# Performance work log

Measured on AMD Instinct MI355X. Metric: run time of the kernel, lower is better.

Reference implementation:

```python
import jax, jax.numpy as jnp
import numpy as np

DIM = 512
HEADS = 8
DIM_HEAD = 64
B, N = 4, 2048
EPS = 1e-5


def setup_inputs() -> dict:
    key = jax.random.key(0)
    ks = jax.random.split(key, 6)
    s = 0.02
    x = jax.random.normal(ks[0], (B, N, DIM), dtype=jnp.float32)
    Wq = jax.random.normal(ks[1], (DIM, HEADS * DIM_HEAD), dtype=jnp.float32) * s
    Wkv = jax.random.normal(ks[2], (DIM, 2 * HEADS * DIM_HEAD), dtype=jnp.float32) * s
    Wo = jax.random.normal(ks[3], (HEADS * DIM_HEAD, DIM), dtype=jnp.float32) * s
    bo = jnp.zeros((DIM,), dtype=jnp.float32)
    # gating layer: torch init is weight=0, bias=1; randomize weight slightly for a nontrivial path
    Wg = jax.random.normal(ks[4], (DIM, HEADS * DIM_HEAD), dtype=jnp.float32) * s
    bg = jnp.ones((HEADS * DIM_HEAD,), dtype=jnp.float32)
    gamma = jnp.ones((DIM,), dtype=jnp.float32)
    beta = jnp.zeros((DIM,), dtype=jnp.float32)
    return {"x": x, "Wq": Wq, "Wkv": Wkv, "Wo": Wo, "bo": bo,
            "Wg": Wg, "bg": bg, "gamma": gamma, "beta": beta}


def reference(x, Wq, Wkv, Wo, bo, Wg, bg, gamma, beta):
    h, d = HEADS, DIM_HEAD
    scale = d ** -0.5
    b, n, _ = x.shape

    q = x @ Wq                                   # [b, n, h*d]
    kv = x @ Wkv                                 # [b, n, 2*h*d]
    k, v = jnp.split(kv, 2, axis=-1)

    def split_heads(t):
        return t.reshape(b, n, h, d).transpose(0, 2, 1, 3)  # [b, h, n, d]

    q = split_heads(q) * scale
    k = split_heads(k)
    v = split_heads(v)

    dots = jnp.einsum('bhid,bhjd->bhij', q, k)   # [b, h, n, n]
    attn = jax.nn.softmax(dots, axis=-1)
    out = jnp.einsum('bhij,bhjd->bhid', attn, v)  # [b, h, n, d]
    out = out.transpose(0, 2, 1, 3).reshape(b, n, h * d)

    gates = x @ Wg + bg                           # [b, n, h*d]
    out = out * jax.nn.sigmoid(gates)
    out = out @ Wo + bo                           # [b, n, dim]
    out = x + out

    # LayerNorm over last dim, eps=1e-5 (torch default)
    mu = jnp.mean(out, axis=-1, keepdims=True)
    var = jnp.var(out, axis=-1, keepdims=True)
    out = (out - mu) * jax.lax.rsqrt(var + EPS) * gamma + beta
    return out
```

## Files before the change

### kernel.cpp

```cpp
#include <hip/hip_runtime.h>
#include <hip/hip_bf16.h>
#include <stdint.h>
#include <stddef.h>

#define SEQ   2048
#define NBATCH 4
#define NHEAD  8
#define DMODEL 512

typedef __attribute__((ext_vector_type(8))) short bf16x8;
typedef __attribute__((ext_vector_type(4))) float f32x4;
typedef __attribute__((ext_vector_type(16))) float f32x16;

#define MFMA16(a, b, c) __builtin_amdgcn_mfma_f32_16x16x32_bf16(a, b, c, 0, 0, 0)
#define MFMA32(a, b, c) __builtin_amdgcn_mfma_f32_32x32x16_bf16(a, b, c, 0, 0, 0)

#define QSCALE 0.18033688011112042f

__device__ __forceinline__ float bf2f(ushort u) {
  union { uint32_t i; float f; } v; v.i = ((uint32_t)u) << 16; return v.f;
}
__device__ __forceinline__ ushort f2bf(float f) {
  union { float f; uint32_t i; } v; v.f = f;
  uint32_t u = v.i;
  return (ushort)((u + 0x7fffu + ((u >> 16) & 1u)) >> 16);
}
__device__ __forceinline__ uint32_t cvtpk(float lo, float hi) {
  uint32_t d;
  asm("v_cvt_pk_bf16_f32 %0, %1, %2" : "=v"(d) : "v"(lo), "v"(hi));
  return d;
}

#if __has_builtin(__builtin_amdgcn_global_load_lds)
__device__ __forceinline__ void gload16(const void* g, void* l) {
  __builtin_amdgcn_global_load_lds(
      (const __attribute__((address_space(1))) void*)g,
      (__attribute__((address_space(3))) void*)l, 16, 0, 0);
}
#define GLOAD_DIRECT 1
#else
#define GLOAD_DIRECT 0
#endif

__global__ __launch_bounds__(256) void cvt_k(const float* __restrict__ in,
                                             ushort* __restrict__ out, int n8) {
  int i = blockIdx.x * 256 + threadIdx.x;
  if (i >= n8) return;
  const float4* p = (const float4*)(in + (size_t)i * 8);
  float4 a = p[0], b = p[1];
  union { int4 v; ushort u[8]; } o;
  o.u[0] = f2bf(a.x); o.u[1] = f2bf(a.y); o.u[2] = f2bf(a.z); o.u[3] = f2bf(a.w);
  o.u[4] = f2bf(b.x); o.u[5] = f2bf(b.y); o.u[6] = f2bf(b.z); o.u[7] = f2bf(b.w);
  *(int4*)(out + (size_t)i * 8) = o.v;
}

__global__ __launch_bounds__(256) void wtrans_k(const float* __restrict__ Wq,
                                                const float* __restrict__ Wkv,
                                                const float* __restrict__ Wg,
                                                const float* __restrict__ Wo,
                                                ushort* __restrict__ WT,
                                                ushort* __restrict__ WoT) {
  __shared__ ushort tile[32][33];
  int bx = blockIdx.x;
  const float* W;
  ushort* dst;
  int N, nt;
  if (bx < 16)       { W = Wq;  dst = WT;              N = 512;  nt = bx; }
  else if (bx < 48)  { W = Wkv; dst = WT + 512 * 512;  N = 1024; nt = bx - 16; }
  else if (bx < 64)  { W = Wg;  dst = WT + 1536 * 512; N = 512;  nt = bx - 48; }
  else               { W = Wo;  dst = WoT;             N = 512;  nt = bx - 64; }
  int t = threadIdx.x;
  int n0 = nt * 32, k0 = blockIdx.y * 32;
  int r = t >> 3, c = (t & 7) * 4;
#pragma unroll
  for (int j = 0; j < 4; j++)
    tile[r][c + j] = f2bf(W[(size_t)(k0 + r) * N + n0 + c + j]);
  __syncthreads();
#pragma unroll
  for (int j = 0; j < 4; j++)
    dst[(size_t)(n0 + r) * 512 + k0 + c + j] = tile[c + j][r];
}

__global__ __launch_bounds__(256, 2) void gemm128_k(const ushort* __restrict__ A,
                                                    const ushort* __restrict__ Bt,
                                                    ushort* __restrict__ qb,
                                                    ushort* __restrict__ kb,
                                                    ushort* __restrict__ vT,
                                                    ushort* __restrict__ gsb,
                                                    const float* __restrict__ bias) {
  __shared__ __align__(16) ushort Sh[4 * 128 * 64];
#define ASB(p) (Sh + (p) * (128 * 64))
#define BSB(p) (Sh + 2 * (128 * 64) + (p) * (128 * 64))
  int t = threadIdx.x;
  int nb = gridDim.x * gridDim.y;
  int bid = blockIdx.y * gridDim.x + blockIdx.x;
  int swz = (bid & 7) * (nb >> 3) + (bid >> 3);
  int row0 = (swz / gridDim.x) * 128, col0 = (swz % gridDim.x) * 128;

  int w = t >> 6, l = t & 63, l31 = l & 31, hi = l >> 5;
  int wm = w >> 1, wn = w & 1;
  f32x16 acc[2][2] = {};

  int srow = t >> 3;
  int ssl = (t & 7) ^ (srow & 7);
  const ushort* Ag = A + (size_t)(row0 + srow) * 512 + ssl * 8;
  const ushort* Bg = Bt + (size_t)(col0 + srow) * 512 + ssl * 8;
  int wslot = __builtin_amdgcn_readfirstlane((t >> 6) << 6);

#if GLOAD_DIRECT
#define STG(p, kt)                                                              \
  do {                                                                          \
    gload16(Ag + (size_t)(kt) * 64 + 0 * 32 * 512, ASB(p) + (wslot +   0) * 8); \
    gload16(Ag + (size_t)(kt) * 64 + 1 * 32 * 512, ASB(p) + (wslot + 256) * 8); \
    gload16(Ag + (size_t)(kt) * 64 + 2 * 32 * 512, ASB(p) + (wslot + 512) * 8); \
    gload16(Ag + (size_t)(kt) * 64 + 3 * 32 * 512, ASB(p) + (wslot + 768) * 8); \
    gload16(Bg + (size_t)(kt) * 64 + 0 * 32 * 512, BSB(p) + (wslot +   0) * 8); \
    gload16(Bg + (size_t)(kt) * 64 + 1 * 32 * 512, BSB(p) + (wslot + 256) * 8); \
    gload16(Bg + (size_t)(kt) * 64 + 2 * 32 * 512, BSB(p) + (wslot + 512) * 8); \
    gload16(Bg + (size_t)(kt) * 64 + 3 * 32 * 512, BSB(p) + (wslot + 768) * 8); \
  } while (0)
#else
#define STG(p, kt)                                                                  \
  do {                                                                              \
    *(int4*)(ASB(p) + (t +   0) * 8) = *(const int4*)(Ag + (size_t)(kt) * 64);      \
    *(int4*)(ASB(p) + (t + 256) * 8) =                                              \
        *(const int4*)(Ag + (size_t)(kt) * 64 + 1 * 32 * 512);                      \
    *(int4*)(ASB(p) + (t + 512) * 8) =                                              \
        *(const int4*)(Ag + (size_t)(kt) * 64 + 2 * 32 * 512);                      \
    *(int4*)(ASB(p) + (t + 768) * 8) =                                              \
        *(const int4*)(Ag + (size_t)(kt) * 64 + 3 * 32 * 512);                      \
    *(int4*)(BSB(p) + (t +   0) * 8) = *(const int4*)(Bg + (size_t)(kt) * 64);      \
    *(int4*)(BSB(p) + (t + 256) * 8) =                                              \
        *(const int4*)(Bg + (size_t)(kt) * 64 + 1 * 32 * 512);                      \
    *(int4*)(BSB(p) + (t + 512) * 8) =                                              \
        *(const int4*)(Bg + (size_t)(kt) * 64 + 2 * 32 * 512);                      \
    *(int4*)(BSB(p) + (t + 768) * 8) =                                              \
        *(const int4*)(Bg + (size_t)(kt) * 64 + 3 * 32 * 512);                      \
  } while (0)
#endif

#define FRAG(Mb, r, s) \
  (*(const bf16x8*)(Mb + ((r) * 64) + ((((s) ^ ((r) & 7))) << 3)))

  STG(0, 0);
  __syncthreads();

  for (int kt = 0; kt < 8; kt++) {
    int p = kt & 1;
    if (kt < 7) STG(p ^ 1, kt + 1);

    bf16x8 bfrag[2][4];
#pragma unroll
    for (int cb = 0; cb < 2; cb++)
#pragma unroll
      for (int kk = 0; kk < 4; kk++)
        bfrag[cb][kk] = FRAG(BSB(p), wn * 64 + cb * 32 + l31, kk * 2 + hi);

    __builtin_amdgcn_s_setprio(1);
#pragma unroll
    for (int rb = 0; rb < 2; rb++) {
      bf16x8 af[4];
#pragma unroll
      for (int kk = 0; kk < 4; kk++)
        af[kk] = FRAG(ASB(p), wm * 64 + rb * 32 + l31, kk * 2 + hi);
#pragma unroll
      for (int kk = 0; kk < 4; kk++) {
        acc[rb][0] = MFMA32(af[kk], bfrag[0][kk], acc[rb][0]);
        acc[rb][1] = MFMA32(af[kk], bfrag[1][kk], acc[rb][1]);
      }
    }
    __builtin_amdgcn_s_setprio(0);

    if (kt < 7) __syncthreads();
  }
#undef STG
#undef FRAG

  if (col0 >= 1024 && col0 < 1536) {
    __syncthreads();
    ushort* lt = Sh;
#pragma unroll
    for (int rb = 0; rb < 2; rb++)
#pragma unroll
      for (int cb = 0; cb < 2; cb++)
#pragma unroll
        for (int e = 0; e < 16; e++) {
          int rr = (e & 3) + 8 * (e >> 2) + 4 * hi;
          int rowL = wm * 64 + rb * 32 + rr;
          int colL = wn * 64 + cb * 32 + l31;
          lt[colL * 136 + rowL] = f2bf(acc[rb][cb][e]);
        }
    __syncthreads();
    int b_ = row0 >> 11;
    int nb0 = row0 & 2047;
#pragma unroll
    for (int r = 0; r < 8; r++) {
      int lin = r * 256 + t;
      int dcol = lin >> 4, n8 = lin & 15;
      int vcol = (col0 - 1024) + dcol;
      int hh = vcol >> 6, dd = vcol & 63;
      bf16x8 v = *(const bf16x8*)(lt + dcol * 136 + n8 * 8);
      *(bf16x8*)(vT + (((size_t)(b_ * 8 + hh) * 64) + dd) * 2048 + nb0 + n8 * 8) = v;
    }
  } else {
#pragma unroll
    for (int rb = 0; rb < 2; rb++) {
#pragma unroll
      for (int cb = 0; cb < 2; cb++) {
#pragma unroll
        for (int e = 0; e < 16; e++) {
          int rr = (e & 3) + 8 * (e >> 2) + 4 * hi;
          int row = row0 + wm * 64 + rb * 32 + rr;
          int col = col0 + wn * 64 + cb * 32 + l31;
          float v = acc[rb][cb][e];
          if (col0 < 512) {
            qb[(size_t)row * 512 + col] = f2bf(v * QSCALE);
          } else if (col0 < 1024) {
            kb[(size_t)row * 512 + (col - 512)] = f2bf(v);
          } else {
            v += bias[col - 1536];
            v = 1.f / (1.f + __expf(-v));
            gsb[(size_t)row * 512 + (col - 1536)] = f2bf(v);
          }
        }
      }
    }
  }
#undef ASB
#undef BSB
}

__global__ __launch_bounds__(256, 2) void gemm_o_k(const ushort* __restrict__ A,
                                                   const ushort* __restrict__ Bt,
                                                   float* __restrict__ yout,
                                                   const float* __restrict__ bias,
                                                   const float* __restrict__ res) {
  __shared__ __align__(16) ushort As[2][128 * 64];
  __shared__ __align__(16) ushort Bs[2][64 * 64];
  int t = threadIdx.x;
  int nb = gridDim.x * gridDim.y;
  int bid = blockIdx.y * gridDim.x + blockIdx.x;
  int swz = (bid & 7) * (nb >> 3) + (bid >> 3);
  int row0 = (swz / gridDim.x) * 128, col0 = (swz % gridDim.x) * 64;

  int w = t >> 6, l = t & 63, l31 = l & 31, hi = l >> 5;
  int wm = w >> 1, wn = w & 1;
  f32x16 acc[2] = {};

  int srow = t >> 3;
  int ssl = (t & 7) ^ (srow & 7);
  const ushort* Ag = A + (size_t)(row0 + srow) * 512 + ssl * 8;
  const ushort* Bg = Bt + (size_t)(col0 + srow) * 512 + ssl * 8;
  int wslot = __builtin_amdgcn_readfirstlane((t >> 6) << 6);

#if GLOAD_DIRECT
#define STG(p, kt)                                                                \
  do {                                                                            \
    gload16(Ag + (size_t)(kt) * 64 + 0 * 32 * 512, &As[p][(wslot +   0) * 8]);    \
    gload16(Ag + (size_t)(kt) * 64 + 1 * 32 * 512, &As[p][(wslot + 256) * 8]);    \
    gload16(Ag + (size_t)(kt) * 64 + 2 * 32 * 512, &As[p][(wslot + 512) * 8]);    \
    gload16(Ag + (size_t)(kt) * 64 + 3 * 32 * 512, &As[p][(wslot + 768) * 8]);    \
    gload16(Bg + (size_t)(kt) * 64 + 0 * 32 * 512, &Bs[p][(wslot +   0) * 8]);    \
    gload16(Bg + (size_t)(kt) * 64 + 1 * 32 * 512, &Bs[p][(wslot + 256) * 8]);    \
  } while (0)
#else
#define STG(p, kt)                                                                  \
  do {                                                                              \
    *(int4*)(&As[p][(t +   0) * 8]) = *(const int4*)(Ag + (size_t)(kt) * 64);       \
    *(int4*)(&As[p][(t + 256) * 8]) =                                               \
        *(const int4*)(Ag + (size_t)(kt) * 64 + 1 * 32 * 512);                      \
    *(int4*)(&As[p][(t + 512) * 8]) =                                               \
        *(const int4*)(Ag + (size_t)(kt) * 64 + 2 * 32 * 512);                      \
    *(int4*)(&As[p][(t + 768) * 8]) =                                               \
        *(const int4*)(Ag + (size_t)(kt) * 64 + 3 * 32 * 512);                      \
    *(int4*)(&Bs[p][(t +   0) * 8]) = *(const int4*)(Bg + (size_t)(kt) * 64);       \
    *(int4*)(&Bs[p][(t + 256) * 8]) =                                               \
        *(const int4*)(Bg + (size_t)(kt) * 64 + 1 * 32 * 512);                      \
  } while (0)
#endif

#define FRAG(Mb, r, s) \
  (*(const bf16x8*)(&(Mb)[((r) * 64) + ((((s) ^ ((r) & 7))) << 3)]))

  STG(0, 0);
  __syncthreads();

  for (int kt = 0; kt < 8; kt++) {
    int p = kt & 1;
    if (kt < 7) STG(p ^ 1, kt + 1);

    bf16x8 bfrag[4];
#pragma unroll
    for (int kk = 0; kk < 4; kk++)
      bfrag[kk] = FRAG(Bs[p], wn * 32 + l31, kk * 2 + hi);

    __builtin_amdgcn_s_setprio(1);
#pragma unroll
    for (int rb = 0; rb < 2; rb++) {
      bf16x8 af[4];
#pragma unroll
      for (int kk = 0; kk < 4; kk++)
        af[kk] = FRAG(As[p], wm * 64 + rb * 32 + l31, kk * 2 + hi);
#pragma unroll
      for (int kk = 0; kk < 4; kk++)
        acc[rb] = MFMA32(af[kk], bfrag[kk], acc[rb]);
    }
    __builtin_amdgcn_s_setprio(0);

    if (kt < 7) __syncthreads();
  }
#undef STG
#undef FRAG

#pragma unroll
  for (int rb = 0; rb < 2; rb++) {
#pragma unroll
    for (int e = 0; e < 16; e++) {
      int rr = (e & 3) + 8 * (e >> 2) + 4 * hi;
      int row = row0 + wm * 64 + rb * 32 + rr;
      int col = col0 + wn * 32 + l31;
      float v = acc[rb][e] + bias[col] + res[(size_t)row * 512 + col];
      yout[(size_t)row * 512 + col] = v;
    }
  }
}

__global__ __launch_bounds__(512) void attn_k(const ushort* __restrict__ q,
                                              const ushort* __restrict__ kbuf,
                                              const ushort* __restrict__ vT,
                                              const ushort* __restrict__ gs,
                                              ushort* __restrict__ gated) {
  __shared__ __align__(16) ushort Kl[2][64][72];
  __shared__ __align__(16) ushort Vl[2][64][72];
  int t = threadIdx.x;
  int bid = blockIdx.x;
  int swz = (bid & 7) * 32 + (bid >> 3);
  int qt = swz & 7, bh = swz >> 3;
  int b = bh >> 3, h = bh & 7;
  int q0 = qt * 256;
  int w = t >> 6, l = t & 63;
  int l31 = l & 31, hi = l >> 5;
  size_t base_n = (size_t)b * SEQ;

  const ushort* qp = q + (base_n + q0 + w * 32 + l31) * 512 + h * 64 + hi * 8;
  bf16x8 qf[4];
#pragma unroll
  for (int kd = 0; kd < 4; kd++)
    qf[kd] = *(const bf16x8*)(qp + kd * 16);

  bf16x8 vones;
#pragma unroll
  for (int j = 0; j < 8; j++) vones[j] = (short)0x3F80;

  f32x16 acco0 = {}, acco1 = {}, acco2 = {};

  int srow = t >> 3, c8 = (t & 7) * 8;
  const ushort* kg = kbuf + (base_n + srow) * 512 + h * 64 + c8;
  const ushort* vg = vT + ((size_t)bh * 64 + srow) * 2048 + c8;

  int4 kA = *(const int4*)(kg);
  int4 vA = *(const int4*)(vg);
  *(int4*)((char*)Kl[0] + srow * 144 + c8 * 2) = kA;
  *(int4*)((char*)Vl[0] + srow * 144 + c8 * 2) = vA;
  kA = *(const int4*)(kg + (size_t)64 * 512);
  vA = *(const int4*)(vg + 64);
  __syncthreads();

  int p = 0;
  for (int jt = 0; jt < SEQ / 64; jt++) {
    f32x16 s0 = {}, s1 = {};
    __builtin_amdgcn_s_setprio(1);
#pragma unroll
    for (int kd = 0; kd < 4; kd++) {
      bf16x8 k0 = *(const bf16x8*)((const char*)Kl[p] + l31 * 144 + kd * 32 + hi * 16);
      bf16x8 k1 = *(const bf16x8*)((const char*)Kl[p] + (32 + l31) * 144 + kd * 32 + hi * 16);
      s0 = MFMA32(k0, qf[kd], s0);
      s1 = MFMA32(k1, qf[kd], s1);
    }
    __builtin_amdgcn_s_setprio(0);

    if (jt < SEQ / 64 - 1) {
      *(int4*)((char*)Kl[p ^ 1] + srow * 144 + c8 * 2) = kA;
      *(int4*)((char*)Vl[p ^ 1] + srow * 144 + c8 * 2) = vA;
    }

    uint32_t pk[16];
#pragma unroll
    for (int sg = 0; sg < 4; sg++) {
#pragma unroll
      for (int u = 0; u < 2; u++) {
        float a = __builtin_amdgcn_exp2f(s0[(sg << 2) | (u << 1)]);
        float c = __builtin_amdgcn_exp2f(s0[(sg << 2) | (u << 1) | 1]);
        pk[sg * 2 + u] = cvtpk(a, c);
      }
    }
#pragma unroll
    for (int sg = 0; sg < 4; sg++) {
#pragma unroll
      for (int u = 0; u < 2; u++) {
        float a = __builtin_amdgcn_exp2f(s1[(sg << 2) | (u << 1)]);
        float c = __builtin_amdgcn_exp2f(s1[(sg << 2) | (u << 1) | 1]);
        pk[8 + sg * 2 + u] = cvtpk(a, c);
      }
    }

    __builtin_amdgcn_s_setprio(1);
#pragma unroll
    for (int jk = 0; jk < 4; jk++) {
      uint32_t x0 = pk[(2 * jk) * 2 + 0], y0 = pk[(2 * jk + 1) * 2 + 0];
      uint32_t x1 = pk[(2 * jk) * 2 + 1], y1 = pk[(2 * jk + 1) * 2 + 1];
      asm("v_permlane32_swap_b32 %0, %1" : "+v"(x0), "+v"(y0));
      asm("v_permlane32_swap_b32 %0, %1" : "+v"(x1), "+v"(y1));
      union { bf16x8 v; uint32_t u[4]; } pa;
      pa.u[0] = x0; pa.u[1] = x1; pa.u[2] = y0; pa.u[3] = y1;
      bf16x8 v0 = *(const bf16x8*)((const char*)Vl[p] + l31 * 144 + jk * 32 + hi * 16);
      bf16x8 v1 = *(const bf16x8*)((const char*)Vl[p] + (32 + l31) * 144 + jk * 32 + hi * 16);
      acco0 = MFMA32(pa.v, v0, acco0);
      acco1 = MFMA32(pa.v, v1, acco1);
      acco2 = MFMA32(pa.v, vones, acco2);
    }
    __builtin_amdgcn_s_setprio(0);

    if (jt < SEQ / 64 - 1) {
      __syncthreads();
      if (jt < SEQ / 64 - 2) {
        kA = *(const int4*)(kg + (size_t)(jt + 2) * 64 * 512);
        vA = *(const int4*)(vg + (jt + 2) * 64);
      }
      p ^= 1;
    }
  }

#pragma unroll
  for (int e = 0; e < 16; e++) {
    int qr = (e & 3) + 8 * (e >> 2) + 4 * hi;
    size_t row = base_n + q0 + w * 32 + qr;
    int col = h * 64 + l31;
    float rcp = 1.f / acco2[e];
    float v0 = acco0[e] * rcp * bf2f(gs[row * 512 + col]);
    float v1 = acco1[e] * rcp * bf2f(gs[row * 512 + col + 32]);
    gated[row * 512 + col] = f2bf(v0);
    gated[row * 512 + col + 32] = f2bf(v1);
  }
}

__global__ __launch_bounds__(256) void ln_k(const float* __restrict__ y,
                                            const float* __restrict__ gamma,
                                            const float* __restrict__ beta,
                                            float* __restrict__ out) {
  int w = threadIdx.x >> 6, l = threadIdx.x & 63;
  size_t row = (size_t)blockIdx.x * 4 + w;
  const float4* yp = (const float4*)(y + row * 512);
  float4 a = yp[l * 2], b = yp[l * 2 + 1];
  float f[8] = {a.x, a.y, a.z, a.w, b.x, b.y, b.z, b.w};
  float sm = 0.f, sq = 0.f;
#pragma unroll
  for (int j = 0; j < 8; j++) { sm += f[j]; sq += f[j] * f[j]; }
#pragma unroll
  for (int off = 1; off < 64; off <<= 1) {
    sm += __shfl_xor(sm, off);
    sq += __shfl_xor(sq, off);
  }
  float mean = sm * (1.f / 512.f);
  float var = sq * (1.f / 512.f) - mean * mean;
  float rs = rsqrtf(var + 1e-5f);
  float4 g0 = ((const float4*)gamma)[l * 2], g1 = ((const float4*)gamma)[l * 2 + 1];
  float4 b0 = ((const float4*)beta)[l * 2],  b1 = ((const float4*)beta)[l * 2 + 1];
  float4 o0, o1;
  o0.x = (f[0] - mean) * rs * g0.x + b0.x;
  o0.y = (f[1] - mean) * rs * g0.y + b0.y;
  o0.z = (f[2] - mean) * rs * g0.z + b0.z;
  o0.w = (f[3] - mean) * rs * g0.w + b0.w;
  o1.x = (f[4] - mean) * rs * g1.x + b1.x;
  o1.y = (f[5] - mean) * rs * g1.y + b1.y;
  o1.z = (f[6] - mean) * rs * g1.z + b1.z;
  o1.w = (f[7] - mean) * rs * g1.w + b1.w;
  float4* op = (float4*)(out + row * 512);
  op[l * 2] = o0;
  op[l * 2 + 1] = o1;
}

extern "C" void kernel_launch(void* const* d_in, const int* in_sizes, int n_in,
                              void* d_out, int out_size, void* d_ws, size_t ws_size,
                              hipStream_t stream) {
  (void)in_sizes; (void)n_in; (void)out_size; (void)ws_size;
  const float* x     = (const float*)d_in[0];
  const float* Wq    = (const float*)d_in[1];
  const float* Wkv   = (const float*)d_in[2];
  const float* Wo    = (const float*)d_in[3];
  const float* bo    = (const float*)d_in[4];
  const float* Wg    = (const float*)d_in[5];
  const float* bg    = (const float*)d_in[6];
  const float* gamma = (const float*)d_in[7];
  const float* beta  = (const float*)d_in[8];

  char* ws = (char*)d_ws;
  ushort* xb    = (ushort*)(ws);
  ushort* qbuf  = (ushort*)(ws + (8u  << 20));
  ushort* kbuf  = (ushort*)(ws + (16u << 20));
  ushort* vT    = (ushort*)(ws + (32u << 20));
  ushort* gsb   = (ushort*)(ws + (40u << 20));
  ushort* gated = (ushort*)(ws + (48u << 20));
  float*  y     = (float*)(ws + (56u << 20));
  ushort* WT    = (ushort*)(ws + (72u << 20));
  ushort* WoT   = (ushort*)(ws + (74u << 20));

  cvt_k<<<(NBATCH * SEQ * DMODEL / 8 + 255) / 256, 256, 0, stream>>>(
      x, xb, NBATCH * SEQ * DMODEL / 8);

  wtrans_k<<<dim3(80, 16), 256, 0, stream>>>(Wq, Wkv, Wg, Wo, WT, WoT);

  gemm128_k<<<dim3(16, 64), 256, 0, stream>>>(xb, WT, qbuf, kbuf, vT, gsb, bg);

  attn_k<<<256, 512, 0, stream>>>(qbuf, kbuf, vT, gsb, gated);

  gemm_o_k<<<dim3(8, 64), 256, 0, stream>>>(gated, WoT, y, bo, x);

  ln_k<<<(NBATCH * SEQ) / 4, 256, 0, stream>>>(y, gamma, beta, (float*)d_out);
}
```

Measured before the change: 114.2 us.

## Merge prep kernels and process 128-key tiles per attention sync

The x conversion and weight transpose kernels are merged into one launch, cutting a kernel launch. The attention loop now stages two 64-key sub-tiles per buffer (128 keys per iteration), halving the number of barriers and global-to-LDS staging rounds. This doubles LDS use per block (about 74 KB) and raises register pressure from holding four prefetch vectors, which could reduce occupancy.

After: 110.6 us (median of 3 runs). 1.03x faster.

```diff
diff --git a/kernel.cpp b/kernel.cpp
--- a/kernel.cpp
+++ b/kernel.cpp
@@ -42,26 +42,28 @@
 #define GLOAD_DIRECT 0
 #endif
 
-__global__ __launch_bounds__(256) void cvt_k(const float* __restrict__ in,
-                                             ushort* __restrict__ out, int n8) {
-  int i = blockIdx.x * 256 + threadIdx.x;
-  if (i >= n8) return;
-  const float4* p = (const float4*)(in + (size_t)i * 8);
-  float4 a = p[0], b = p[1];
-  union { int4 v; ushort u[8]; } o;
-  o.u[0] = f2bf(a.x); o.u[1] = f2bf(a.y); o.u[2] = f2bf(a.z); o.u[3] = f2bf(a.w);
-  o.u[4] = f2bf(b.x); o.u[5] = f2bf(b.y); o.u[6] = f2bf(b.z); o.u[7] = f2bf(b.w);
-  *(int4*)(out + (size_t)i * 8) = o.v;
-}
-
-__global__ __launch_bounds__(256) void wtrans_k(const float* __restrict__ Wq,
-                                                const float* __restrict__ Wkv,
-                                                const float* __restrict__ Wg,
-                                                const float* __restrict__ Wo,
-                                                ushort* __restrict__ WT,
-                                                ushort* __restrict__ WoT) {
+__global__ __launch_bounds__(256) void prep_k(const float* __restrict__ x,
+                                              const float* __restrict__ Wq,
+                                              const float* __restrict__ Wkv,
+                                              const float* __restrict__ Wg,
+                                              const float* __restrict__ Wo,
+                                              ushort* __restrict__ xb,
+                                              ushort* __restrict__ WT,
+                                              ushort* __restrict__ WoT) {
   __shared__ ushort tile[32][33];
-  int bx = blockIdx.x;
+  int t = threadIdx.x;
+  if (blockIdx.x < 2048) {
+    int i = blockIdx.x * 256 + t;
+    const float4* p = (const float4*)(x + (size_t)i * 8);
+    float4 a = p[0], b = p[1];
+    union { int4 v; ushort u[8]; } o;
+    o.u[0] = f2bf(a.x); o.u[1] = f2bf(a.y); o.u[2] = f2bf(a.z); o.u[3] = f2bf(a.w);
+    o.u[4] = f2bf(b.x); o.u[5] = f2bf(b.y); o.u[6] = f2bf(b.z); o.u[7] = f2bf(b.w);
+    *(int4*)(xb + (size_t)i * 8) = o.v;
+    return;
+  }
+  int bidx = blockIdx.x - 2048;
+  int bx = bidx % 80, by = bidx / 80;
   const float* W;
   ushort* dst;
   int N, nt;
@@ -69,8 +71,7 @@
   else if (bx < 48)  { W = Wkv; dst = WT + 512 * 512;  N = 1024; nt = bx - 16; }
   else if (bx < 64)  { W = Wg;  dst = WT + 1536 * 512; N = 512;  nt = bx - 48; }
   else               { W = Wo;  dst = WoT;             N = 512;  nt = bx - 64; }
-  int t = threadIdx.x;
-  int n0 = nt * 32, k0 = blockIdx.y * 32;
+  int n0 = nt * 32, k0 = by * 32;
   int r = t >> 3, c = (t & 7) * 4;
 #pragma unroll
   for (int j = 0; j < 4; j++)
@@ -330,8 +331,8 @@
                                               const ushort* __restrict__ vT,
                                               const ushort* __restrict__ gs,
                                               ushort* __restrict__ gated) {
-  __shared__ __align__(16) ushort Kl[2][64][72];
-  __shared__ __align__(16) ushort Vl[2][64][72];
+  __shared__ __align__(16) ushort Kl[2][2][64][72];
+  __shared__ __align__(16) ushort Vl[2][2][64][72];
   int t = threadIdx.x;
   int bid = blockIdx.x;
   int swz = (bid & 7) * 32 + (bid >> 3);
@@ -358,78 +359,117 @@
   const ushort* kg = kbuf + (base_n + srow) * 512 + h * 64 + c8;
   const ushort* vg = vT + ((size_t)bh * 64 + srow) * 2048 + c8;
 
-  int4 kA = *(const int4*)(kg);
-  int4 vA = *(const int4*)(vg);
-  *(int4*)((char*)Kl[0] + srow * 144 + c8 * 2) = kA;
-  *(int4*)((char*)Vl[0] + srow * 144 + c8 * 2) = vA;
-  kA = *(const int4*)(kg + (size_t)64 * 512);
-  vA = *(const int4*)(vg + 64);
+#define QK_PHASE(KB, S0, S1)                                                   \
+  do {                                                                         \
+    _Pragma("unroll")                                                          \
+    for (int kd = 0; kd < 4; kd++) {                                           \
+      bf16x8 k0 = *(const bf16x8*)((KB) + l31 * 144 + kd * 32 + hi * 16);      \
+      bf16x8 k1 = *(const bf16x8*)((KB) + (32 + l31) * 144 + kd * 32 + hi * 16);\
+      S0 = MFMA32(k0, qf[kd], S0);                                             \
+      S1 = MFMA32(k1, qf[kd], S1);                                             \
+    }                                                                          \
+  } while (0)
+
+#define SM_PHASE(S0, S1, PK)                                                   \
+  do {                                                                         \
+    _Pragma("unroll")                                                          \
+    for (int sg = 0; sg < 4; sg++) {                                           \
+      _Pragma("unroll")                                                        \
+      for (int u = 0; u < 2; u++) {                                            \
+        float a = __builtin_amdgcn_exp2f(S0[(sg << 2) | (u << 1)]);            \
+        float c = __builtin_amdgcn_exp2f(S0[(sg << 2) | (u << 1) | 1]);        \
+        PK[sg * 2 + u] = cvtpk(a, c);                                          \
+      }                                                                        \
+    }                                                                          \
+    _Pragma("unroll")                                                          \
+    for (int sg = 0; sg < 4; sg++) {                                           \
+      _Pragma("unroll")                                                        \
+      for (int u = 0; u < 2; u++) {                                            \
+        float a = __builtin_amdgcn_exp2f(S1[(sg << 2) | (u << 1)]);            \
+        float c = __builtin_amdgcn_exp2f(S1[(sg << 2) | (u << 1) | 1]);        \
+        PK[8 + sg * 2 + u] = cvtpk(a, c);                                      \
+      }                                                                        \
+    }                                                                          \
+  } while (0)
+
+#define PV_PHASE(VB, PK)                                                       \
+  do {                                                                         \
+    _Pragma("unroll")                                                          \
+    for (int jk = 0; jk < 4; jk++) {                                           \
+      uint32_t x0 = PK[(2 * jk) * 2 + 0], y0 = PK[(2 * jk + 1) * 2 + 0];       \
+      uint32_t x1 = PK[(2 * jk) * 2 + 1], y1 = PK[(2 * jk + 1) * 2 + 1];       \
+      asm("v_permlane32_swap_b32 %0, %1" : "+v"(x0), "+v"(y0));                \
+      asm("v_permlane32_swap_b32 %0, %1" : "+v"(x1), "+v"(y1));                \
+      union { bf16x8 v; uint32_t u[4]; } pa;                                   \
+      pa.u[0] = x0; pa.u[1] = x1; pa.u[2] = y0; pa.u[3] = y1;                  \
+      bf16x8 v0 = *(const bf16x8*)((VB) + l31 * 144 + jk * 32 + hi * 16);      \
+      bf16x8 v1 = *(const bf16x8*)((VB) + (32 + l31) * 144 + jk * 32 + hi * 16);\
+      acco0 = MFMA32(pa.v, v0, acco0);                                         \
+      acco1 = MFMA32(pa.v, v1, acco1);                                         \
+      acco2 = MFMA32(pa.v, vones, acco2);                                      \
+    }                                                                          \
+  } while (0)
+
+#define STAGE_LDS(pp)                                                          \
+  do {                                                                         \
+    *(int4*)((char*)Kl[pp][0] + srow * 144 + c8 * 2) = kA;                     \
+    *(int4*)((char*)Kl[pp][1] + srow * 144 + c8 * 2) = kB;                     \
+    *(int4*)((char*)Vl[pp][0] + srow * 144 + c8 * 2) = vA;                     \
+    *(int4*)((char*)Vl[pp][1] + srow * 144 + c8 * 2) = vB;                     \
+  } while (0)
+
+#define LOADT(n)                                                               \
+  do {                                                                         \
+    kA = *(const int4*)(kg + (size_t)(n) * 128 * 512);                         \
+    kB = *(const int4*)(kg + ((size_t)(n) * 128 + 64) * 512);                  \
+    vA = *(const int4*)(vg + (n) * 128);                                       \
+    vB = *(const int4*)(vg + (n) * 128 + 64);                                  \
+  } while (0)
+
+  int4 kA, kB, vA, vB;
+  LOADT(0);
+  STAGE_LDS(0);
+  LOADT(1);
   __syncthreads();
 
   int p = 0;
-  for (int jt = 0; jt < SEQ / 64; jt++) {
+  const int NT = SEQ / 128;
+  for (int jt = 0; jt < NT; jt++) {
     f32x16 s0 = {}, s1 = {};
     __builtin_amdgcn_s_setprio(1);
-#pragma unroll
-    for (int kd = 0; kd < 4; kd++) {
-      bf16x8 k0 = *(const bf16x8*)((const char*)Kl[p] + l31 * 144 + kd * 32 + hi * 16);
-      bf16x8 k1 = *(const bf16x8*)((const char*)Kl[p] + (32 + l31) * 144 + kd * 32 + hi * 16);
-      s0 = MFMA32(k0, qf[kd], s0);
-      s1 = MFMA32(k1, qf[kd], s1);
-    }
+    QK_PHASE((const char*)Kl[p][0], s0, s1);
     __builtin_amdgcn_s_setprio(0);
-
-    if (jt < SEQ / 64 - 1) {
-      *(int4*)((char*)Kl[p ^ 1] + srow * 144 + c8 * 2) = kA;
-      *(int4*)((char*)Vl[p ^ 1] + srow * 144 + c8 * 2) = vA;
-    }
-
-    uint32_t pk[16];
-#pragma unroll
-    for (int sg = 0; sg < 4; sg++) {
-#pragma unroll
-      for (int u = 0; u < 2; u++) {
-        float a = __builtin_amdgcn_exp2f(s0[(sg << 2) | (u << 1)]);
-        float c = __builtin_amdgcn_exp2f(s0[(sg << 2) | (u << 1) | 1]);
-        pk[sg * 2 + u] = cvtpk(a, c);
-      }
-    }
-#pragma unroll
-    for (int sg = 0; sg < 4; sg++) {
-#pragma unroll
-      for (int u = 0; u < 2; u++) {
-        float a = __builtin_amdgcn_exp2f(s1[(sg << 2) | (u << 1)]);
-        float c = __builtin_amdgcn_exp2f(s1[(sg << 2) | (u << 1) | 1]);
-        pk[8 + sg * 2 + u] = cvtpk(a, c);
-      }
-    }
-
+    if (jt < NT - 1) STAGE_LDS(p ^ 1);
+    {
+      uint32_t pk[16];
+      SM_PHASE(s0, s1, pk);
+      __builtin_amdgcn_s_setprio(1);
+      PV_PHASE((const char*)Vl[p][0], pk);
+      __builtin_amdgcn_s_setprio(0);
+    }
+    s0 = (f32x16){}; s1 = (f32x16){};
     __builtin_amdgcn_s_setprio(1);
-#pragma unroll
-    for (int jk = 0; jk < 4; jk++) {
-      uint32_t x0 = pk[(2 * jk) * 2 + 0], y0 = pk[(2 * jk + 1) * 2 + 0];
-      uint32_t x1 = pk[(2 * jk) * 2 + 1], y1 = pk[(2 * jk + 1) * 2 + 1];
-      asm("v_permlane32_swap_b32 %0, %1" : "+v"(x0), "+v"(y0));
-      asm("v_permlane32_swap_b32 %0, %1" : "+v"(x1), "+v"(y1));
-      union { bf16x8 v; uint32_t u[4]; } pa;
-      pa.u[0] = x0; pa.u[1] = x1; pa.u[2] = y0; pa.u[3] = y1;
-      bf16x8 v0 = *(const bf16x8*)((const char*)Vl[p] + l31 * 144 + jk * 32 + hi * 16);
-      bf16x8 v1 = *(const bf16x8*)((const char*)Vl[p] + (32 + l31) * 144 + jk * 32 + hi * 16);
-      acco0 = MFMA32(pa.v, v0, acco0);
-      acco1 = MFMA32(pa.v, v1, acco1);
-      acco2 = MFMA32(pa.v, vones, acco2);
-    }
+    QK_PHASE((const char*)Kl[p][1], s0, s1);
     __builtin_amdgcn_s_setprio(0);
-
-    if (jt < SEQ / 64 - 1) {
+    {
+      uint32_t pk[16];
+      SM_PHASE(s0, s1, pk);
+      __builtin_amdgcn_s_setprio(1);
+      PV_PHASE((const char*)Vl[p][1], pk);
+      __builtin_amdgcn_s_setprio(0);
+    }
+
+    if (jt < NT - 1) {
       __syncthreads();
-      if (jt < SEQ / 64 - 2) {
-        kA = *(const int4*)(kg + (size_t)(jt + 2) * 64 * 512);
-        vA = *(const int4*)(vg + (jt + 2) * 64);
-      }
+      if (jt < NT - 2) LOADT(jt + 2);
       p ^= 1;
     }
   }
+#undef QK_PHASE
+#undef SM_PHASE
+#undef PV_PHASE
+#undef STAGE_LDS
+#undef LOADT
 
 #pragma unroll
   for (int e = 0; e < 16; e++) {
@@ -505,10 +545,7 @@
   ushort* WT    = (ushort*)(ws + (72u << 20));
   ushort* WoT   = (ushort*)(ws + (74u << 20));
 
-  cvt_k<<<(NBATCH * SEQ * DMODEL / 8 + 255) / 256, 256, 0, stream>>>(
-      x, xb, NBATCH * SEQ * DMODEL / 8);
-
-  wtrans_k<<<dim3(80, 16), 256, 0, stream>>>(Wq, Wkv, Wg, Wo, WT, WoT);
+  prep_k<<<2048 + 1280, 256, 0, stream>>>(x, Wq, Wkv, Wg, Wo, xb, WT, WoT);
 
   gemm128_k<<<dim3(16, 64), 256, 0, stream>>>(xb, WT, qbuf, kbuf, vT, gsb, bg);
 
```
